# Optimization experiments

Measured on AMD Instinct MI355X. Metric: run time of the kernel, lower is better.

The kernel has to match this reference:

```python
import jax, jax.numpy as jnp
import numpy as np

N = 262144
C = 256
G = 4096  # number of segments (upper bound on group ids)


def setup_inputs() -> dict:
    key = jax.random.key(0)
    ks = jax.random.split(key, 8)
    s = 1.0 / np.sqrt(C)
    x = jax.random.normal(ks[0], (1, N, C), dtype=jnp.float32)
    ix = jax.random.randint(ks[1], (N,), 0, G, dtype=jnp.int64)
    Wf = jax.random.uniform(ks[2], (C, C), jnp.float32, -s, s)
    bf = jax.random.uniform(ks[3], (C,), jnp.float32, -s, s)
    Wg = jax.random.uniform(ks[4], (C, C), jnp.float32, -s, s)
    bg = jax.random.uniform(ks[5], (C,), jnp.float32, -s, s)
    Wh = jax.random.uniform(ks[6], (C, C), jnp.float32, -s, s)
    bh = jax.random.uniform(ks[7], (C,), jnp.float32, -s, s)
    return {"x": x, "Wf": Wf, "bf": bf, "Wg": Wg, "bg": bg, "Wh": Wh, "bh": bh, "ix": ix}


def reference(x, Wf, bf, Wg, bg, Wh, bh, ix):
    # x: [1, N, C]; only batch 0 is used (matches torch module)
    x0 = x[0]                                    # [N, C]
    fx = x0 @ Wf.T + bf                          # [N, C]
    gx = jnp.clip(x0 @ Wg.T + bg, -50.0, 50.0)   # [N, C]
    exp_gx = jnp.exp(gx)                         # [N, C]
    # Segment softmax: sorting + cumsum group relabel in the torch code is
    # mathematically just a per-group normalized weighted sum keyed by ix.
    seg = ix.astype(jnp.int32)
    denom = jax.ops.segment_sum(exp_gx, seg, num_segments=G)   # [G, C]
    w = exp_gx / denom[seg]                                    # [N, C]
    y = jax.ops.segment_sum(fx * w, seg, num_segments=G)       # [G, C]
    y = y @ Wh.T + bh                                          # [G, C]
    out = y[seg]                                               # [N, C]
    return out[None]                                           # [1, N, C]
```

## Files before the change

kernel.cpp:

```cpp
#include <hip/hip_runtime.h>
#include <stdint.h>
#include <stddef.h>

#define N_ROWS 262144
#define CCH    256
#define NGRP   4096

typedef short bf16x8 __attribute__((ext_vector_type(8)));
typedef short bf16x4 __attribute__((ext_vector_type(4)));
typedef float f32x4  __attribute__((ext_vector_type(4)));
typedef float f32x16 __attribute__((ext_vector_type(16)));

static __device__ __forceinline__ short f2bf(float f){
  union { float f; unsigned u; } v; v.f = f;
  unsigned u = v.u;
  unsigned r = (u + 0x7FFFu + ((u >> 16) & 1u)) >> 16;
  return (short)r;
}

typedef __attribute__((address_space(1))) const unsigned int GU32;
typedef __attribute__((address_space(3))) unsigned int LU32;
static __device__ __forceinline__ void gload_lds16(const void* g, void* l){
  __builtin_amdgcn_global_load_lds((GU32*)g, (LU32*)l, 16, 0, 0);
}

__global__ __launch_bounds__(256) void k_castw(
    const float* __restrict__ Wf, const float* __restrict__ Wg,
    const float* __restrict__ Wh,
    short* __restrict__ wfb, short* __restrict__ wgb, float* __restrict__ wht)
{
  int e = blockIdx.x * 256 + threadIdx.x;
  wfb[e] = f2bf(Wf[e]);
  wgb[e] = f2bf(Wg[e]);
  int k = e >> 8, j = e & 255;
  wht[e] = Wh[j * 256 + k];
}

__global__ __launch_bounds__(256) void k_hist(const int* __restrict__ ix, int* __restrict__ counts){
  int i = blockIdx.x * blockDim.x + threadIdx.x;
  int stride = gridDim.x * blockDim.x;
  for (; i < N_ROWS; i += stride) atomicAdd(&counts[ix[i]], 1);
}

__global__ __launch_bounds__(1024) void k_scan(const int* __restrict__ counts, int* __restrict__ cursor){
  __shared__ int sums[1024];
  int t = threadIdx.x;
  int base = t * 4;
  int c0 = counts[base], c1 = counts[base+1], c2 = counts[base+2], c3 = counts[base+3];
  sums[t] = c0 + c1 + c2 + c3;
  __syncthreads();
  for (int off = 1; off < 1024; off <<= 1){
    int v = (t >= off) ? sums[t - off] : 0;
    __syncthreads();
    sums[t] += v;
    __syncthreads();
  }
  int prev = (t == 0) ? 0 : sums[t - 1];
  cursor[base]   = prev;
  cursor[base+1] = prev + c0;
  cursor[base+2] = prev + c0 + c1;
  cursor[base+3] = prev + c0 + c1 + c2;
}

__global__ __launch_bounds__(256) void k_scatter_cast(
    const int* __restrict__ ix, int* __restrict__ cursor,
    const float* __restrict__ x, short* __restrict__ xb, int* __restrict__ gid)
{
  int wave = threadIdx.x >> 6;
  int lane = threadIdx.x & 63;
  int i = blockIdx.x * 4 + wave;
  int stride = gridDim.x * 4;
  for (; i < N_ROWS; i += stride){
    int g = ix[i];
    int p;
    if (lane == 0) p = atomicAdd(&cursor[g], 1);
    p = __shfl(p, 0);
    f32x4 v = *(const f32x4*)(x + (size_t)i * 256 + lane * 4);
    bf16x4 b;
    #pragma unroll
    for (int j = 0; j < 4; ++j) b[j] = f2bf(v[j]);
    *(bf16x4*)(xb + (size_t)p * 256 + lane * 4) = b;
    if (lane == 0) gid[p] = g;
  }
}

__global__ __launch_bounds__(256) void k_gemm(
    const short* __restrict__ xb,
    const short* __restrict__ wfb, const short* __restrict__ wgb,
    const float* __restrict__ bfp, const float* __restrict__ bgp,
    const int* __restrict__ gid,
    float* __restrict__ numer, float* __restrict__ denom)
{
  __shared__ short bst[32][512];

  const int tid  = threadIdx.x;
  const int wave = tid >> 6;
  const int lane = tid & 63;
  const int l31  = lane & 31;
  const int hi   = lane >> 5;

  const int p     = blockIdx.x;
  const int xcd   = p & 7;
  const int ixd   = p >> 3;
  const int cg    = ixd & 7;
  const int bslot = xcd * 32 + (ixd >> 3);
  const int j0    = cg * 32;

  #pragma unroll
  for (int q = 0; q < 8; ++q){
    int f = wave * 8 + q;
    int mat = f >> 4, ks = f & 15;
    const short* wsrc = mat ? wgb : wfb;
    const short* src = wsrc + (size_t)(j0 + l31) * 256 + ks * 16 + hi * 8;
    gload_lds16(src, &bst[f][0]);
  }
  __syncthreads();

  const float bfv = bfp[j0 + l31];
  const float bgv = bgp[j0 + l31];

  for (int tile = bslot; tile < N_ROWS / 128; tile += 256){
    const int row0 = tile * 128 + wave * 32;
    const int gidv = gid[row0 + l31];
    const short* xr = xb + (size_t)(row0 + l31) * 256 + hi * 8;

    f32x16 accF, accG;
    #pragma unroll
    for (int r = 0; r < 16; ++r){ accF[r] = 0.f; accG[r] = 0.f; }

    #pragma unroll
    for (int ks = 0; ks < 16; ++ks){
      bf16x8 a  = *(const bf16x8*)(xr + ks * 16);
      bf16x8 bF = *(const bf16x8*)&bst[ks][lane * 8];
      bf16x8 bG = *(const bf16x8*)&bst[16 + ks][lane * 8];
      __builtin_amdgcn_s_setprio(1);
      accF = __builtin_amdgcn_mfma_f32_32x32x16_bf16(a, bF, accF, 0, 0, 0);
      accG = __builtin_amdgcn_mfma_f32_32x32x16_bf16(a, bG, accG, 0, 0, 0);
      __builtin_amdgcn_s_setprio(0);
    }

    #pragma unroll
    for (int r = 0; r < 16; ++r){
      float g = accG[r] + bgv;
      g = fminf(fmaxf(g, -50.f), 50.f);
      float e = __expf(g);
      accF[r] = (accF[r] + bfv) * e;
      accG[r] = e;
    }

    int gprev = __shfl(gidv, (l31 + 31) & 31);
    bool head = (l31 == 0) || (gidv != gprev);
    unsigned long long hb = __ballot(head) & 0xFFFFFFFFull;
    int start = 0;
    while (start < 32){
      int g = __shfl(gidv, start);
      unsigned long long rest = hb >> (start + 1);
      int end = rest ? (start + 1 + __builtin_ctzll(rest)) : 32;
      float sF = 0.f, sE = 0.f;
      #pragma unroll
      for (int r = 0; r < 16; ++r){
        int row = (r & 3) + 8 * (r >> 2) + 4 * hi;
        bool in = (row >= start) && (row < end);
        sF += in ? accF[r] : 0.f;
        sE += in ? accG[r] : 0.f;
      }
      sF += __shfl_xor(sF, 32);
      sE += __shfl_xor(sE, 32);
      if (hi == 0){
        atomicAdd(&numer[(size_t)g * 256 + j0 + l31], sF);
        atomicAdd(&denom[(size_t)g * 256 + j0 + l31], sE);
      }
      start = end;
    }
  }
}

__global__ __launch_bounds__(256) void k_yh(
    const float* __restrict__ numer, const float* __restrict__ denom,
    const float* __restrict__ wht, const float* __restrict__ bh,
    float* __restrict__ yh)
{
  __shared__ float ys[16][256];
  int t = threadIdx.x;
  int g0 = blockIdx.x * 16;
  #pragma unroll
  for (int gg = 0; gg < 16; ++gg){
    size_t idx = (size_t)(g0 + gg) * 256 + t;
    float d = denom[idx];
    ys[gg][t] = (d != 0.f) ? (numer[idx] / d) : 0.f;
  }
  __syncthreads();
  float acc[16];
  #pragma unroll
  for (int gg = 0; gg < 16; ++gg) acc[gg] = 0.f;
  for (int k = 0; k < 256; k += 4){
    float w0 = wht[(k+0) * 256 + t];
    float w1 = wht[(k+1) * 256 + t];
    float w2 = wht[(k+2) * 256 + t];
    float w3 = wht[(k+3) * 256 + t];
    #pragma unroll
    for (int gg = 0; gg < 16; ++gg)
      acc[gg] += w0 * ys[gg][k] + w1 * ys[gg][k+1] + w2 * ys[gg][k+2] + w3 * ys[gg][k+3];
  }
  float b = bh[t];
  #pragma unroll
  for (int gg = 0; gg < 16; ++gg) yh[(size_t)(g0 + gg) * 256 + t] = acc[gg] + b;
}

__global__ __launch_bounds__(256) void k_out(const int* __restrict__ ix,
    const float* __restrict__ yh, float* __restrict__ out)
{
  int wave = threadIdx.x >> 6;
  int lane = threadIdx.x & 63;
  int i = blockIdx.x * 4 + wave;
  int stride = gridDim.x * 4;
  for (; i < N_ROWS; i += stride){
    int g = ix[i];
    f32x4 v = *(const f32x4*)(yh + (size_t)g * 256 + lane * 4);
    *(f32x4*)(out + (size_t)i * 256 + lane * 4) = v;
  }
}

extern "C" void kernel_launch(void* const* d_in, const int* in_sizes, int n_in,
                              void* d_out, int out_size, void* d_ws, size_t ws_size,
                              hipStream_t stream)
{
  const float* x  = (const float*)d_in[0];
  const float* Wf = (const float*)d_in[1];
  const float* bf = (const float*)d_in[2];
  const float* Wg = (const float*)d_in[3];
  const float* bg = (const float*)d_in[4];
  const float* Wh = (const float*)d_in[5];
  const float* bh = (const float*)d_in[6];
  const int*   ix = (const int*)d_in[7];
  float* out = (float*)d_out;

  char* ws = (char*)d_ws;
  float* numer  = (float*)(ws + 0);
  float* denom  = (float*)(ws + 4194304);
  int*   counts = (int*)  (ws + 8388608);
  int*   cursor = (int*)  (ws + 8404992);
  float* yh     = (float*)(ws + 8421376);
  float* wht    = (float*)(ws + 12615680);
  short* wfb    = (short*)(ws + 12877824);
  short* wgb    = (short*)(ws + 13008896);
  int*   gid    = (int*)  (ws + 13139968);

  short* xb = (short*)d_out;

  hipMemsetAsync(ws, 0, 8404992, stream);

  k_castw<<<256, 256, 0, stream>>>(Wf, Wg, Wh, wfb, wgb, wht);
  k_hist<<<512, 256, 0, stream>>>(ix, counts);
  k_scan<<<1, 1024, 0, stream>>>(counts, cursor);
  k_scatter_cast<<<2048, 256, 0, stream>>>(ix, cursor, x, xb, gid);
  k_gemm<<<2048, 256, 0, stream>>>(xb, wfb, wgb, bf, bg, gid, numer, denom);
  k_yh<<<256, 256, 0, stream>>>(numer, denom, wht, bh, yh);
  k_out<<<2048, 256, 0, stream>>>(ix, yh, out);
}
```

Measured before the change: 794.1 us.

## Software-pipeline A-operand loads in segment GEMM and fast-path single-group tiles

Restructures the k_gemm tile loop so the MFMA k-steps are interleaved with batches of global loads of later A fragments. It also prefetches the next tile's first four fragments and its group ids during the current tile's compute, to hide global memory latency behind matrix work. A fast path handles 32-row slices that belong to a single group and skips the masked segment loop. The trip count is hardcoded to 8, and more live registers could lower occupancy.

```diff
diff --git a/kernel.cpp b/kernel.cpp
--- a/kernel.cpp
+++ b/kernel.cpp
@@ -119,25 +119,54 @@
   const float bfv = bfp[j0 + l31];
   const float bgv = bgp[j0 + l31];
 
-  for (int tile = bslot; tile < N_ROWS / 128; tile += 256){
-    const int row0 = tile * 128 + wave * 32;
-    const int gidv = gid[row0 + l31];
-    const short* xr = xb + (size_t)(row0 + l31) * 256 + hi * 8;
+#define KSTEP(A, KS) do { \
+    bf16x8 bF_ = *(const bf16x8*)&bst[(KS)][lane * 8]; \
+    accF = __builtin_amdgcn_mfma_f32_32x32x16_bf16((A), bF_, accF, 0, 0, 0); \
+    bf16x8 bG_ = *(const bf16x8*)&bst[16 + (KS)][lane * 8]; \
+    accG = __builtin_amdgcn_mfma_f32_32x32x16_bf16((A), bG_, accG, 0, 0, 0); \
+  } while (0)
+
+  int tile = bslot;
+  const short* xr = xb + (size_t)(tile * 128 + wave * 32 + l31) * 256 + hi * 8;
+  int gidv = gid[tile * 128 + wave * 32 + l31];
+  bf16x8 p0 = *(const bf16x8*)(xr + 0 * 16);
+  bf16x8 p1 = *(const bf16x8*)(xr + 1 * 16);
+  bf16x8 p2 = *(const bf16x8*)(xr + 2 * 16);
+  bf16x8 p3 = *(const bf16x8*)(xr + 3 * 16);
+
+  #pragma unroll 1
+  for (int it = 0; it < 8; ++it){
+    const int tnext = (it < 7) ? tile + 256 : tile;
+    const int rown  = tnext * 128 + wave * 32 + l31;
+    const short* xrn = xb + (size_t)rown * 256 + hi * 8;
 
     f32x16 accF, accG;
     #pragma unroll
     for (int r = 0; r < 16; ++r){ accF[r] = 0.f; accG[r] = 0.f; }
 
-    #pragma unroll
-    for (int ks = 0; ks < 16; ++ks){
-      bf16x8 a  = *(const bf16x8*)(xr + ks * 16);
-      bf16x8 bF = *(const bf16x8*)&bst[ks][lane * 8];
-      bf16x8 bG = *(const bf16x8*)&bst[16 + ks][lane * 8];
-      __builtin_amdgcn_s_setprio(1);
-      accF = __builtin_amdgcn_mfma_f32_32x32x16_bf16(a, bF, accF, 0, 0, 0);
-      accG = __builtin_amdgcn_mfma_f32_32x32x16_bf16(a, bG, accG, 0, 0, 0);
-      __builtin_amdgcn_s_setprio(0);
-    }
+    bf16x8 a4 = *(const bf16x8*)(xr + 4 * 16);
+    bf16x8 a5 = *(const bf16x8*)(xr + 5 * 16);
+    bf16x8 a6 = *(const bf16x8*)(xr + 6 * 16);
+    bf16x8 a7 = *(const bf16x8*)(xr + 7 * 16);
+    __builtin_amdgcn_s_setprio(1);
+    KSTEP(p0, 0); KSTEP(p1, 1); KSTEP(p2, 2); KSTEP(p3, 3);
+    bf16x8 a8  = *(const bf16x8*)(xr + 8 * 16);
+    bf16x8 a9  = *(const bf16x8*)(xr + 9 * 16);
+    bf16x8 a10 = *(const bf16x8*)(xr + 10 * 16);
+    bf16x8 a11 = *(const bf16x8*)(xr + 11 * 16);
+    KSTEP(a4, 4); KSTEP(a5, 5); KSTEP(a6, 6); KSTEP(a7, 7);
+    bf16x8 a12 = *(const bf16x8*)(xr + 12 * 16);
+    bf16x8 a13 = *(const bf16x8*)(xr + 13 * 16);
+    bf16x8 a14 = *(const bf16x8*)(xr + 14 * 16);
+    bf16x8 a15 = *(const bf16x8*)(xr + 15 * 16);
+    KSTEP(a8, 8); KSTEP(a9, 9); KSTEP(a10, 10); KSTEP(a11, 11);
+    int gidn = gid[rown];
+    bf16x8 n0 = *(const bf16x8*)(xrn + 0 * 16);
+    bf16x8 n1 = *(const bf16x8*)(xrn + 1 * 16);
+    bf16x8 n2 = *(const bf16x8*)(xrn + 2 * 16);
+    bf16x8 n3 = *(const bf16x8*)(xrn + 3 * 16);
+    KSTEP(a12, 12); KSTEP(a13, 13); KSTEP(a14, 14); KSTEP(a15, 15);
+    __builtin_amdgcn_s_setprio(0);
 
     #pragma unroll
     for (int r = 0; r < 16; ++r){
@@ -151,28 +180,45 @@
     int gprev = __shfl(gidv, (l31 + 31) & 31);
     bool head = (l31 == 0) || (gidv != gprev);
     unsigned long long hb = __ballot(head) & 0xFFFFFFFFull;
-    int start = 0;
-    while (start < 32){
-      int g = __shfl(gidv, start);
-      unsigned long long rest = hb >> (start + 1);
-      int end = rest ? (start + 1 + __builtin_ctzll(rest)) : 32;
+    if (hb == 1ull){
+      int g = __shfl(gidv, 0);
       float sF = 0.f, sE = 0.f;
       #pragma unroll
-      for (int r = 0; r < 16; ++r){
-        int row = (r & 3) + 8 * (r >> 2) + 4 * hi;
-        bool in = (row >= start) && (row < end);
-        sF += in ? accF[r] : 0.f;
-        sE += in ? accG[r] : 0.f;
-      }
+      for (int r = 0; r < 16; ++r){ sF += accF[r]; sE += accG[r]; }
       sF += __shfl_xor(sF, 32);
       sE += __shfl_xor(sE, 32);
       if (hi == 0){
         atomicAdd(&numer[(size_t)g * 256 + j0 + l31], sF);
         atomicAdd(&denom[(size_t)g * 256 + j0 + l31], sE);
       }
-      start = end;
+    } else {
+      int start = 0;
+      while (start < 32){
+        int g = __shfl(gidv, start);
+        unsigned long long rest = hb >> (start + 1);
+        int end = rest ? (start + 1 + __builtin_ctzll(rest)) : 32;
+        float sF = 0.f, sE = 0.f;
+        #pragma unroll
+        for (int r = 0; r < 16; ++r){
+          int row = (r & 3) + 8 * (r >> 2) + 4 * hi;
+          bool in = (row >= start) && (row < end);
+          sF += in ? accF[r] : 0.f;
+          sE += in ? accG[r] : 0.f;
+        }
+        sF += __shfl_xor(sF, 32);
+        sE += __shfl_xor(sE, 32);
+        if (hi == 0){
+          atomicAdd(&numer[(size_t)g * 256 + j0 + l31], sF);
+          atomicAdd(&denom[(size_t)g * 256 + j0 + l31], sE);
+        }
+        start = end;
+      }
     }
-  }
+
+    p0 = n0; p1 = n1; p2 = n2; p3 = n3;
+    gidv = gidn; xr = xrn; tile = tnext;
+  }
+#undef KSTEP
 }
 
 __global__ __launch_bounds__(256) void k_yh(
```

After: 718.1 us. 1.11x faster.

## Software-pipeline A loads in gemm, fast-path uniform segments, sorted-order output gather

Applied to the files above, without the earlier changes.

The GEMM inner loop is restructured to prefetch A fragments in two register banks, overlapping global loads with MFMAs, and the per-tile loop is kept rolled. A fast path handles tiles whose 32 rows all share one group, skipping the masked per-segment reduction loop. The output kernel now walks rows in sorted order, recording the original index during scatter, so consecutive waves read the same yh row for better cache locality, though output writes become scattered.

```diff
diff --git a/kernel.cpp b/kernel.cpp
--- a/kernel.cpp
+++ b/kernel.cpp
@@ -64,7 +64,8 @@
 
 __global__ __launch_bounds__(256) void k_scatter_cast(
     const int* __restrict__ ix, int* __restrict__ cursor,
-    const float* __restrict__ x, short* __restrict__ xb, int* __restrict__ gid)
+    const float* __restrict__ x, short* __restrict__ xb,
+    int* __restrict__ gid, int* __restrict__ order)
 {
   int wave = threadIdx.x >> 6;
   int lane = threadIdx.x & 63;
@@ -80,7 +81,7 @@
     #pragma unroll
     for (int j = 0; j < 4; ++j) b[j] = f2bf(v[j]);
     *(bf16x4*)(xb + (size_t)p * 256 + lane * 4) = b;
-    if (lane == 0) gid[p] = g;
+    if (lane == 0){ gid[p] = g; order[p] = i; }
   }
 }
 
@@ -119,6 +120,14 @@
   const float bfv = bfp[j0 + l31];
   const float bgv = bgp[j0 + l31];
 
+#define KSTEP(A, KS) do { \
+    bf16x8 bF_ = *(const bf16x8*)&bst[(KS)][lane * 8]; \
+    accF = __builtin_amdgcn_mfma_f32_32x32x16_bf16((A), bF_, accF, 0, 0, 0); \
+    bf16x8 bG_ = *(const bf16x8*)&bst[16 + (KS)][lane * 8]; \
+    accG = __builtin_amdgcn_mfma_f32_32x32x16_bf16((A), bG_, accG, 0, 0, 0); \
+  } while (0)
+
+  #pragma unroll 1
   for (int tile = bslot; tile < N_ROWS / 128; tile += 256){
     const int row0 = tile * 128 + wave * 32;
     const int gidv = gid[row0 + l31];
@@ -128,16 +137,28 @@
     #pragma unroll
     for (int r = 0; r < 16; ++r){ accF[r] = 0.f; accG[r] = 0.f; }
 
-    #pragma unroll
-    for (int ks = 0; ks < 16; ++ks){
-      bf16x8 a  = *(const bf16x8*)(xr + ks * 16);
-      bf16x8 bF = *(const bf16x8*)&bst[ks][lane * 8];
-      bf16x8 bG = *(const bf16x8*)&bst[16 + ks][lane * 8];
-      __builtin_amdgcn_s_setprio(1);
-      accF = __builtin_amdgcn_mfma_f32_32x32x16_bf16(a, bF, accF, 0, 0, 0);
-      accG = __builtin_amdgcn_mfma_f32_32x32x16_bf16(a, bG, accG, 0, 0, 0);
-      __builtin_amdgcn_s_setprio(0);
-    }
+    bf16x8 a0 = *(const bf16x8*)(xr + 0 * 16);
+    bf16x8 a1 = *(const bf16x8*)(xr + 1 * 16);
+    bf16x8 a2 = *(const bf16x8*)(xr + 2 * 16);
+    bf16x8 a3 = *(const bf16x8*)(xr + 3 * 16);
+    bf16x8 b0 = *(const bf16x8*)(xr + 4 * 16);
+    bf16x8 b1 = *(const bf16x8*)(xr + 5 * 16);
+    bf16x8 b2 = *(const bf16x8*)(xr + 6 * 16);
+    bf16x8 b3 = *(const bf16x8*)(xr + 7 * 16);
+    __builtin_amdgcn_s_setprio(1);
+    KSTEP(a0, 0); KSTEP(a1, 1); KSTEP(a2, 2); KSTEP(a3, 3);
+    a0 = *(const bf16x8*)(xr + 8 * 16);
+    a1 = *(const bf16x8*)(xr + 9 * 16);
+    a2 = *(const bf16x8*)(xr + 10 * 16);
+    a3 = *(const bf16x8*)(xr + 11 * 16);
+    KSTEP(b0, 4); KSTEP(b1, 5); KSTEP(b2, 6); KSTEP(b3, 7);
+    b0 = *(const bf16x8*)(xr + 12 * 16);
+    b1 = *(const bf16x8*)(xr + 13 * 16);
+    b2 = *(const bf16x8*)(xr + 14 * 16);
+    b3 = *(const bf16x8*)(xr + 15 * 16);
+    KSTEP(a0, 8); KSTEP(a1, 9); KSTEP(a2, 10); KSTEP(a3, 11);
+    KSTEP(b0, 12); KSTEP(b1, 13); KSTEP(b2, 14); KSTEP(b3, 15);
+    __builtin_amdgcn_s_setprio(0);
 
     #pragma unroll
     for (int r = 0; r < 16; ++r){
@@ -151,28 +172,42 @@
     int gprev = __shfl(gidv, (l31 + 31) & 31);
     bool head = (l31 == 0) || (gidv != gprev);
     unsigned long long hb = __ballot(head) & 0xFFFFFFFFull;
-    int start = 0;
-    while (start < 32){
-      int g = __shfl(gidv, start);
-      unsigned long long rest = hb >> (start + 1);
-      int end = rest ? (start + 1 + __builtin_ctzll(rest)) : 32;
+    if (hb == 1ull){
+      int g = __shfl(gidv, 0);
       float sF = 0.f, sE = 0.f;
       #pragma unroll
-      for (int r = 0; r < 16; ++r){
-        int row = (r & 3) + 8 * (r >> 2) + 4 * hi;
-        bool in = (row >= start) && (row < end);
-        sF += in ? accF[r] : 0.f;
-        sE += in ? accG[r] : 0.f;
-      }
+      for (int r = 0; r < 16; ++r){ sF += accF[r]; sE += accG[r]; }
       sF += __shfl_xor(sF, 32);
       sE += __shfl_xor(sE, 32);
       if (hi == 0){
         atomicAdd(&numer[(size_t)g * 256 + j0 + l31], sF);
         atomicAdd(&denom[(size_t)g * 256 + j0 + l31], sE);
       }
-      start = end;
+    } else {
+      int start = 0;
+      while (start < 32){
+        int g = __shfl(gidv, start);
+        unsigned long long rest = hb >> (start + 1);
+        int end = rest ? (start + 1 + __builtin_ctzll(rest)) : 32;
+        float sF = 0.f, sE = 0.f;
+        #pragma unroll
+        for (int r = 0; r < 16; ++r){
+          int row = (r & 3) + 8 * (r >> 2) + 4 * hi;
+          bool in = (row >= start) && (row < end);
+          sF += in ? accF[r] : 0.f;
+          sE += in ? accG[r] : 0.f;
+        }
+        sF += __shfl_xor(sF, 32);
+        sE += __shfl_xor(sE, 32);
+        if (hi == 0){
+          atomicAdd(&numer[(size_t)g * 256 + j0 + l31], sF);
+          atomicAdd(&denom[(size_t)g * 256 + j0 + l31], sE);
+        }
+        start = end;
+      }
     }
   }
+#undef KSTEP
 }
 
 __global__ __launch_bounds__(256) void k_yh(
@@ -207,17 +242,18 @@
   for (int gg = 0; gg < 16; ++gg) yh[(size_t)(g0 + gg) * 256 + t] = acc[gg] + b;
 }
 
-__global__ __launch_bounds__(256) void k_out(const int* __restrict__ ix,
-    const float* __restrict__ yh, float* __restrict__ out)
+__global__ __launch_bounds__(256) void k_out(const int* __restrict__ order,
+    const int* __restrict__ gid, const float* __restrict__ yh, float* __restrict__ out)
 {
   int wave = threadIdx.x >> 6;
   int lane = threadIdx.x & 63;
-  int i = blockIdx.x * 4 + wave;
+  int pidx = blockIdx.x * 4 + wave;
   int stride = gridDim.x * 4;
-  for (; i < N_ROWS; i += stride){
-    int g = ix[i];
+  for (; pidx < N_ROWS; pidx += stride){
+    int g = gid[pidx];
+    int dst = order[pidx];
     f32x4 v = *(const f32x4*)(yh + (size_t)g * 256 + lane * 4);
-    *(f32x4*)(out + (size_t)i * 256 + lane * 4) = v;
+    *(f32x4*)(out + (size_t)dst * 256 + lane * 4) = v;
   }
 }
 
@@ -245,6 +281,7 @@
   short* wfb    = (short*)(ws + 12877824);
   short* wgb    = (short*)(ws + 13008896);
   int*   gid    = (int*)  (ws + 13139968);
+  int*   order  = (int*)  (ws + 14188544);
 
   short* xb = (short*)d_out;
 
@@ -253,8 +290,8 @@
   k_castw<<<256, 256, 0, stream>>>(Wf, Wg, Wh, wfb, wgb, wht);
   k_hist<<<512, 256, 0, stream>>>(ix, counts);
   k_scan<<<1, 1024, 0, stream>>>(counts, cursor);
-  k_scatter_cast<<<2048, 256, 0, stream>>>(ix, cursor, x, xb, gid);
+  k_scatter_cast<<<2048, 256, 0, stream>>>(ix, cursor, x, xb, gid, order);
   k_gemm<<<2048, 256, 0, stream>>>(xb, wfb, wgb, bf, bg, gid, numer, denom);
   k_yh<<<256, 256, 0, stream>>>(numer, denom, wht, bh, yh);
-  k_out<<<2048, 256, 0, stream>>>(ix, yh, out);
-}
+  k_out<<<2048, 256, 0, stream>>>(order, gid, yh, out);
+}
```

After: 722.8 us. 1.1x faster.
